# Performance work log

Measured on AMD Instinct MI355X. Metric: run time of the kernel, lower is better.

The kernel has to match this reference:

```python
import jax, jax.numpy as jnp
import numpy as np

NUM_HEADS = 8
WINDOW = 8


def setup_inputs() -> dict:
    key = jax.random.key(0)
    k1, k2, k3, k4 = jax.random.split(key, 4)
    B, H, W, C = 8, 192, 192, 192
    x = jax.random.normal(k1, (B, H * W, C), dtype=jnp.float32)
    w_qkv = jax.random.normal(k2, (C, 3 * C), dtype=jnp.float32) * 0.02
    w_proj = jax.random.normal(k3, (C, C), dtype=jnp.float32) * 0.02
    b_proj = jax.random.normal(k4, (C,), dtype=jnp.float32) * 0.02
    return {"x": x, "w_qkv": w_qkv, "w_proj": w_proj, "b_proj": b_proj, "H": H, "W": W}


def reference(x, w_qkv, w_proj, b_proj, H, W):
    B, L, C = x.shape
    N = WINDOW * WINDOW  # 64 tokens per window
    Nw = L // N          # number of windows (torch view chain == flat reshape, no permute)
    scale = (C // NUM_HEADS) ** -0.5
    # qkv projection on flat tokens, then window reshape
    qkv = (x @ w_qkv).reshape(B, Nw, N, 3, C)
    q = qkv[..., 0, :]
    k = qkv[..., 1, :] * scale
    v = qkv[..., 2, :]
    # channel attention: [B,Nw,C,C]
    attn = jnp.einsum('bwnc,bwnd->bwcd', k, v)
    attn = jax.nn.softmax(attn, axis=-1)
    # out[b,w,n,c] = sum_d attn[b,w,c,d] * q[b,w,n,d]
    out = jnp.einsum('bwcd,bwnd->bwnc', attn, q)
    out = out.reshape(B, L, C)
    return out @ w_proj + b_proj
```

## Files before the change

### kernel.cpp

```cpp
#include <hip/hip_runtime.h>
#include <hip/hip_bf16.h>

typedef short bf16x8 __attribute__((ext_vector_type(8)));
typedef float f32x4  __attribute__((ext_vector_type(4)));

__device__ __forceinline__ unsigned short f2bf(float f) {
  unsigned int u = __float_as_uint(f);
  u += 0x7fffu + ((u >> 16) & 1u);
  return (unsigned short)(u >> 16);
}

__device__ __forceinline__ f32x4 fzero() { f32x4 z = {0.f, 0.f, 0.f, 0.f}; return z; }

#define WQKV_FRAGS (6*36*64)
#define WP_FRAGS   (6*12*64)
#define WQKV_ELEMS (WQKV_FRAGS*8)

__global__ void prepack_weights(const float* __restrict__ wqkv,
                                const float* __restrict__ wproj,
                                unsigned short* __restrict__ ws) {
  int t = blockIdx.x * 256 + threadIdx.x;
  const float scale = 0.20412414523193154f;
  if (t < WQKV_FRAGS) {
    int kt  = t / (36*64);
    int rem = t - kt*(36*64);
    int nt  = rem >> 6;
    int l   = rem & 63;
    int n   = nt*16 + (l & 15);
    int k0  = kt*32 + (l >> 4)*8;
    float s = (n >= 192 && n < 384) ? scale : 1.0f;
    union { unsigned short us[8]; uint4 v; } u;
#pragma unroll
    for (int j = 0; j < 8; ++j) u.us[j] = f2bf(wqkv[(k0 + j)*576 + n] * s);
    *(uint4*)(ws + (size_t)t * 8) = u.v;
  } else if (t < WQKV_FRAGS + WP_FRAGS) {
    int t2  = t - WQKV_FRAGS;
    int kt  = t2 / (12*64);
    int rem = t2 - kt*(12*64);
    int nt  = rem >> 6;
    int l   = rem & 63;
    int n   = nt*16 + (l & 15);
    int k0  = kt*32 + (l >> 4)*8;
    union { unsigned short us[8]; uint4 v; } u;
#pragma unroll
    for (int j = 0; j < 8; ++j) u.us[j] = f2bf(wproj[(k0 + j)*192 + n]);
    *(uint4*)(ws + (size_t)WQKV_ELEMS + (size_t)t2 * 8) = u.v;
  }
}

__launch_bounds__(512, 2)
__global__ void win_attn_fused(const float* __restrict__ x,
                               const unsigned short* __restrict__ wqkv_sw,
                               const unsigned short* __restrict__ wp_sw,
                               const float* __restrict__ bias,
                               float* __restrict__ out) {
  __shared__ __align__(16) unsigned char smem[156672];
  unsigned short* sX    = (unsigned short*)(smem);
  unsigned short* sQ    = (unsigned short*)(smem + 25600);
  unsigned short* sKt   = (unsigned short*)(smem + 51200);
  unsigned short* sVt   = (unsigned short*)(smem + 78848);
  float*          sAttn = (float*)(smem + 106496);
  unsigned short* sOut  = (unsigned short*)(smem);

  const int tid  = threadIdx.x;
  const int lane = tid & 63;
  const int wv   = tid >> 6;
  const int l16  = lane & 15;
  const int lq   = lane >> 4;

  {
    const float4* xg = (const float4*)(x + (size_t)blockIdx.x * 12288);
#pragma unroll
    for (int i = 0; i < 6; ++i) {
      int idx = tid + i * 512;
      float4 v = xg[idx];
      int e = idx << 2;
      unsigned short* p = sX + (e / 192) * 200 + (e % 192);
      p[0] = f2bf(v.x); p[1] = f2bf(v.y); p[2] = f2bf(v.z); p[3] = f2bf(v.w);
    }
  }
  __syncthreads();

  {
    bf16x8 af[4][6];
#pragma unroll
    for (int ms = 0; ms < 4; ++ms)
#pragma unroll
      for (int kt = 0; kt < 6; ++kt)
        af[ms][kt] = *(const bf16x8*)(sX + (ms*16 + l16)*200 + kt*32 + lq*8);

    for (int nt = wv; nt < 36; nt += 8) {
      f32x4 acc[4] = {fzero(), fzero(), fzero(), fzero()};
      const bf16x8* bp = (const bf16x8*)wqkv_sw + nt*64 + lane;
#pragma unroll
      for (int kt = 0; kt < 6; ++kt) {
        bf16x8 b = bp[kt * (36*64)];
#pragma unroll
        for (int ms = 0; ms < 4; ++ms)
          acc[ms] = __builtin_amdgcn_mfma_f32_16x16x32_bf16(af[ms][kt], b, acc[ms], 0, 0, 0);
      }
      int c = nt*16 + l16;
#pragma unroll
      for (int ms = 0; ms < 4; ++ms) {
        int rb = ms*16 + lq*4;
        if (c < 192) {
#pragma unroll
          for (int r = 0; r < 4; ++r) sQ[(rb + r)*200 + c] = f2bf(acc[ms][r]);
        } else if (c < 384) {
#pragma unroll
          for (int r = 0; r < 4; ++r) sKt[(c - 192)*72 + rb + r] = f2bf(acc[ms][r]);
        } else {
#pragma unroll
          for (int r = 0; r < 4; ++r) sVt[(c - 384)*72 + rb + r] = f2bf(acc[ms][r]);
        }
      }
    }
  }
  __syncthreads();

  f32x4 accF[2][4];
#pragma unroll
  for (int s = 0; s < 2; ++s)
#pragma unroll
    for (int m = 0; m < 4; ++m) accF[s][m] = fzero();

  for (int cb = 0; cb < 3; ++cb) {
    {
      bf16x8 ak[4][2];
#pragma unroll
      for (int ms = 0; ms < 4; ++ms)
#pragma unroll
        for (int kt = 0; kt < 2; ++kt)
          ak[ms][kt] = *(const bf16x8*)(sKt + (cb*64 + ms*16 + l16)*72 + kt*32 + lq*8);
      for (int dt = wv; dt < 12; dt += 8) {
        f32x4 acc[4] = {fzero(), fzero(), fzero(), fzero()};
#pragma unroll
        for (int kt = 0; kt < 2; ++kt) {
          bf16x8 b = *(const bf16x8*)(sVt + (dt*16 + l16)*72 + kt*32 + lq*8);
#pragma unroll
          for (int ms = 0; ms < 4; ++ms)
            acc[ms] = __builtin_amdgcn_mfma_f32_16x16x32_bf16(ak[ms][kt], b, acc[ms], 0, 0, 0);
        }
        int d = dt*16 + l16;
#pragma unroll
        for (int ms = 0; ms < 4; ++ms)
#pragma unroll
          for (int r = 0; r < 4; ++r)
            sAttn[(ms*16 + lq*4 + r)*196 + d] = acc[ms][r];
      }
    }
    __syncthreads();

    {
      int row = tid >> 3, seg = tid & 7;
      float* rp = sAttn + row*196 + seg*24;
      float v0[24];
      float mx = -3.0e38f;
#pragma unroll
      for (int i = 0; i < 24; ++i) { v0[i] = rp[i]; mx = fmaxf(mx, v0[i]); }
      mx = fmaxf(mx, __shfl_xor(mx, 1));
      mx = fmaxf(mx, __shfl_xor(mx, 2));
      mx = fmaxf(mx, __shfl_xor(mx, 4));
      float s = 0.f;
#pragma unroll
      for (int i = 0; i < 24; ++i) { float e = __expf(v0[i] - mx); v0[i] = e; s += e; }
      s += __shfl_xor(s, 1);
      s += __shfl_xor(s, 2);
      s += __shfl_xor(s, 4);
      float inv = 1.0f / s;
#pragma unroll
      for (int i = 0; i < 24; ++i) rp[i] = v0[i] * inv;
    }
    __syncthreads();

    {
      int ct = wv & 3, mh = wv >> 2;
      bf16x8 aq[2][6];
#pragma unroll
      for (int mi = 0; mi < 2; ++mi)
#pragma unroll
        for (int kt = 0; kt < 6; ++kt)
          aq[mi][kt] = *(const bf16x8*)(sQ + ((mh*2 + mi)*16 + l16)*200 + kt*32 + lq*8);
      f32x4 acc[2] = {fzero(), fzero()};
#pragma unroll
      for (int kt = 0; kt < 6; ++kt) {
        const float* ap = sAttn + (ct*16 + l16)*196 + kt*32 + lq*8;
        float4 f0 = *(const float4*)ap;
        float4 f1 = *(const float4*)(ap + 4);
        bf16x8 b;
        b[0] = (short)f2bf(f0.x); b[1] = (short)f2bf(f0.y);
        b[2] = (short)f2bf(f0.z); b[3] = (short)f2bf(f0.w);
        b[4] = (short)f2bf(f1.x); b[5] = (short)f2bf(f1.y);
        b[6] = (short)f2bf(f1.z); b[7] = (short)f2bf(f1.w);
#pragma unroll
        for (int mi = 0; mi < 2; ++mi)
          acc[mi] = __builtin_amdgcn_mfma_f32_16x16x32_bf16(aq[mi][kt], b, acc[mi], 0, 0, 0);
      }
#pragma unroll
      for (int mi = 0; mi < 2; ++mi)
#pragma unroll
        for (int r = 0; r < 4; ++r)
          sOut[((mh*2 + mi)*16 + lq*4 + r)*72 + ct*16 + l16] = f2bf(acc[mi][r]);
    }
    __syncthreads();

    {
      bf16x8 ao[4][2];
#pragma unroll
      for (int ms = 0; ms < 4; ++ms)
#pragma unroll
        for (int kt = 0; kt < 2; ++kt)
          ao[ms][kt] = *(const bf16x8*)(sOut + (ms*16 + l16)*72 + kt*32 + lq*8);
#pragma unroll
      for (int slot = 0; slot < 2; ++slot) {
        int nt = wv + slot*8;
        if (nt < 12) {
          const bf16x8* bp = (const bf16x8*)wp_sw + ((cb*2)*12 + nt)*64 + lane;
#pragma unroll
          for (int kt = 0; kt < 2; ++kt) {
            bf16x8 b = bp[kt * (12*64)];
#pragma unroll
            for (int ms = 0; ms < 4; ++ms)
              accF[slot][ms] = __builtin_amdgcn_mfma_f32_16x16x32_bf16(ao[ms][kt], b, accF[slot][ms], 0, 0, 0);
          }
        }
      }
    }
  }

  {
    float* op = out + (size_t)blockIdx.x * 12288;
#pragma unroll
    for (int slot = 0; slot < 2; ++slot) {
      int nt = wv + slot*8;
      if (nt < 12) {
        int e = nt*16 + l16;
        float bv = bias[e];
#pragma unroll
        for (int ms = 0; ms < 4; ++ms)
#pragma unroll
          for (int r = 0; r < 4; ++r)
            op[(ms*16 + lq*4 + r)*192 + e] = accF[slot][ms][r] + bv;
      }
    }
  }
}

extern "C" void kernel_launch(void* const* d_in, const int* in_sizes, int n_in,
                              void* d_out, int out_size, void* d_ws, size_t ws_size,
                              hipStream_t stream) {
  const float* x     = (const float*)d_in[0];
  const float* wqkv  = (const float*)d_in[1];
  const float* wproj = (const float*)d_in[2];
  const float* bproj = (const float*)d_in[3];
  unsigned short* ws = (unsigned short*)d_ws;

  int nwin = in_sizes[0] / 12288;

  prepack_weights<<<72, 256, 0, stream>>>(wqkv, wproj, ws);
  win_attn_fused<<<nwin, 512, 0, stream>>>(x, ws, ws + WQKV_ELEMS, bproj, (float*)d_out);
}
```

Before: 591.2 us.

## Restructure channel attention into single pass with deferred softmax normalization

Replaces the three-chunk loop over channel blocks with one pass. Each wave computes a 96x48 slice of the K^T V scores in registers, exponentiates them without max subtraction, and produces row sums via shuffles and a small shared reduction. The 1/sum scale is applied after the attention-times-Q product. That product is shuffled straight into MFMA fragments for the output projection, with the two halves combined in shared memory and written out as coalesced float4 stores. This cuts shared-memory traffic, the fp32 attention buffer and barriers, and shrinks LDS. Dropping the max subtraction risks exp overflow for large logits.

Result: no change. 599.8 us (+1.5%).

```diff
diff --git a/kernel.cpp b/kernel.cpp
--- a/kernel.cpp
+++ b/kernel.cpp
@@ -1,5 +1,4 @@
 #include <hip/hip_runtime.h>
-#include <hip/hip_bf16.h>
 
 typedef short bf16x8 __attribute__((ext_vector_type(8)));
 typedef float f32x4  __attribute__((ext_vector_type(4)));
@@ -9,8 +8,8 @@
   u += 0x7fffu + ((u >> 16) & 1u);
   return (unsigned short)(u >> 16);
 }
-
-__device__ __forceinline__ f32x4 fzero() { f32x4 z = {0.f, 0.f, 0.f, 0.f}; return z; }
+__device__ __forceinline__ short f2bfs(float f) { return (short)f2bf(f); }
+__device__ __forceinline__ f32x4 fzero() { f32x4 z = {0.f,0.f,0.f,0.f}; return z; }
 
 #define WQKV_FRAGS (6*36*64)
 #define WP_FRAGS   (6*12*64)
@@ -22,8 +21,8 @@
   int t = blockIdx.x * 256 + threadIdx.x;
   const float scale = 0.20412414523193154f;
   if (t < WQKV_FRAGS) {
-    int kt  = t / (36*64);
-    int rem = t - kt*(36*64);
+    int kt  = t / 2304;
+    int rem = t - kt*2304;
     int nt  = rem >> 6;
     int l   = rem & 63;
     int n   = nt*16 + (l & 15);
@@ -34,16 +33,16 @@
     for (int j = 0; j < 8; ++j) u.us[j] = f2bf(wqkv[(k0 + j)*576 + n] * s);
     *(uint4*)(ws + (size_t)t * 8) = u.v;
   } else if (t < WQKV_FRAGS + WP_FRAGS) {
-    int t2  = t - WQKV_FRAGS;
-    int kt  = t2 / (12*64);
-    int rem = t2 - kt*(12*64);
-    int nt  = rem >> 6;
-    int l   = rem & 63;
-    int n   = nt*16 + (l & 15);
-    int k0  = kt*32 + (l >> 4)*8;
+    int t2   = t - WQKV_FRAGS;
+    int kt2g = t2 / 768;
+    int rem  = t2 - kt2g*768;
+    int ms2  = rem >> 6;
+    int l    = rem & 63;
+    int e    = ms2*16 + (l & 15);
+    int cc0  = kt2g*32 + (l >> 4)*8;
     union { unsigned short us[8]; uint4 v; } u;
 #pragma unroll
-    for (int j = 0; j < 8; ++j) u.us[j] = f2bf(wproj[(k0 + j)*192 + n]);
+    for (int j = 0; j < 8; ++j) u.us[j] = f2bf(wproj[(cc0 + j)*192 + e]);
     *(uint4*)(ws + (size_t)WQKV_ELEMS + (size_t)t2 * 8) = u.v;
   }
 }
@@ -54,20 +53,26 @@
                                const unsigned short* __restrict__ wp_sw,
                                const float* __restrict__ bias,
                                float* __restrict__ out) {
-  __shared__ __align__(16) unsigned char smem[156672];
-  unsigned short* sX    = (unsigned short*)(smem);
-  unsigned short* sQ    = (unsigned short*)(smem + 25600);
-  unsigned short* sKt   = (unsigned short*)(smem + 51200);
-  unsigned short* sVt   = (unsigned short*)(smem + 78848);
-  float*          sAttn = (float*)(smem + 106496);
-  unsigned short* sOut  = (unsigned short*)(smem);
+  __shared__ __align__(16) unsigned char smem[107264];
+  unsigned short* sX   = (unsigned short*)(smem);
+  unsigned short* sKt  = (unsigned short*)(smem + 25600);
+  unsigned short* sVt  = (unsigned short*)(smem + 53248);
+  unsigned short* sQ   = (unsigned short*)(smem + 80896);
+  unsigned short* sAtt = (unsigned short*)(smem);
+  float* sSum  = (float*)(smem + 76800);
+  float* sInv  = (float*)(smem + 79872);
+  float* sEpi  = (float*)(smem);
+  float* sBias = (float*)(smem + 106496);
 
   const int tid  = threadIdx.x;
   const int lane = tid & 63;
   const int wv   = tid >> 6;
   const int l16  = lane & 15;
   const int lq   = lane >> 4;
-
+  const int h    = wv >> 2;
+  const int q    = wv & 3;
+
+  if (tid < 192) sBias[tid] = bias[tid];
   {
     const float4* xg = (const float4*)(x + (size_t)blockIdx.x * 12288);
 #pragma unroll
@@ -76,7 +81,9 @@
       float4 v = xg[idx];
       int e = idx << 2;
       unsigned short* p = sX + (e / 192) * 200 + (e % 192);
-      p[0] = f2bf(v.x); p[1] = f2bf(v.y); p[2] = f2bf(v.z); p[3] = f2bf(v.w);
+      union { unsigned short us[4]; unsigned long long d; } u;
+      u.us[0]=f2bf(v.x); u.us[1]=f2bf(v.y); u.us[2]=f2bf(v.z); u.us[3]=f2bf(v.w);
+      *(unsigned long long*)p = u.d;
     }
   }
   __syncthreads();
@@ -94,7 +101,7 @@
       const bf16x8* bp = (const bf16x8*)wqkv_sw + nt*64 + lane;
 #pragma unroll
       for (int kt = 0; kt < 6; ++kt) {
-        bf16x8 b = bp[kt * (36*64)];
+        bf16x8 b = bp[kt * 2304];
 #pragma unroll
         for (int ms = 0; ms < 4; ++ms)
           acc[ms] = __builtin_amdgcn_mfma_f32_16x16x32_bf16(af[ms][kt], b, acc[ms], 0, 0, 0);
@@ -118,130 +125,160 @@
   }
   __syncthreads();
 
-  f32x4 accF[2][4];
-#pragma unroll
-  for (int s = 0; s < 2; ++s)
-#pragma unroll
-    for (int m = 0; m < 4; ++m) accF[s][m] = fzero();
-
-  for (int cb = 0; cb < 3; ++cb) {
-    {
-      bf16x8 ak[4][2];
-#pragma unroll
-      for (int ms = 0; ms < 4; ++ms)
-#pragma unroll
-        for (int kt = 0; kt < 2; ++kt)
-          ak[ms][kt] = *(const bf16x8*)(sKt + (cb*64 + ms*16 + l16)*72 + kt*32 + lq*8);
-      for (int dt = wv; dt < 12; dt += 8) {
-        f32x4 acc[4] = {fzero(), fzero(), fzero(), fzero()};
-#pragma unroll
-        for (int kt = 0; kt < 2; ++kt) {
-          bf16x8 b = *(const bf16x8*)(sVt + (dt*16 + l16)*72 + kt*32 + lq*8);
-#pragma unroll
-          for (int ms = 0; ms < 4; ++ms)
-            acc[ms] = __builtin_amdgcn_mfma_f32_16x16x32_bf16(ak[ms][kt], b, acc[ms], 0, 0, 0);
-        }
-        int d = dt*16 + l16;
-#pragma unroll
-        for (int ms = 0; ms < 4; ++ms)
-#pragma unroll
-          for (int r = 0; r < 4; ++r)
-            sAttn[(ms*16 + lq*4 + r)*196 + d] = acc[ms][r];
-      }
-    }
-    __syncthreads();
-
-    {
-      int row = tid >> 3, seg = tid & 7;
-      float* rp = sAttn + row*196 + seg*24;
-      float v0[24];
-      float mx = -3.0e38f;
-#pragma unroll
-      for (int i = 0; i < 24; ++i) { v0[i] = rp[i]; mx = fmaxf(mx, v0[i]); }
-      mx = fmaxf(mx, __shfl_xor(mx, 1));
-      mx = fmaxf(mx, __shfl_xor(mx, 2));
-      mx = fmaxf(mx, __shfl_xor(mx, 4));
-      float s = 0.f;
-#pragma unroll
-      for (int i = 0; i < 24; ++i) { float e = __expf(v0[i] - mx); v0[i] = e; s += e; }
-      s += __shfl_xor(s, 1);
-      s += __shfl_xor(s, 2);
-      s += __shfl_xor(s, 4);
-      float inv = 1.0f / s;
-#pragma unroll
-      for (int i = 0; i < 24; ++i) rp[i] = v0[i] * inv;
-    }
-    __syncthreads();
-
-    {
-      int ct = wv & 3, mh = wv >> 2;
-      bf16x8 aq[2][6];
-#pragma unroll
-      for (int mi = 0; mi < 2; ++mi)
-#pragma unroll
-        for (int kt = 0; kt < 6; ++kt)
-          aq[mi][kt] = *(const bf16x8*)(sQ + ((mh*2 + mi)*16 + l16)*200 + kt*32 + lq*8);
-      f32x4 acc[2] = {fzero(), fzero()};
-#pragma unroll
-      for (int kt = 0; kt < 6; ++kt) {
-        const float* ap = sAttn + (ct*16 + l16)*196 + kt*32 + lq*8;
-        float4 f0 = *(const float4*)ap;
-        float4 f1 = *(const float4*)(ap + 4);
-        bf16x8 b;
-        b[0] = (short)f2bf(f0.x); b[1] = (short)f2bf(f0.y);
-        b[2] = (short)f2bf(f0.z); b[3] = (short)f2bf(f0.w);
-        b[4] = (short)f2bf(f1.x); b[5] = (short)f2bf(f1.y);
-        b[6] = (short)f2bf(f1.z); b[7] = (short)f2bf(f1.w);
-#pragma unroll
-        for (int mi = 0; mi < 2; ++mi)
-          acc[mi] = __builtin_amdgcn_mfma_f32_16x16x32_bf16(aq[mi][kt], b, acc[mi], 0, 0, 0);
-      }
-#pragma unroll
-      for (int mi = 0; mi < 2; ++mi)
+  f32x4 acc2[6][3];
+  float p24[24];
+  {
+    bf16x8 ak[6][2];
+#pragma unroll
+    for (int ms = 0; ms < 6; ++ms)
+#pragma unroll
+      for (int kt = 0; kt < 2; ++kt)
+        ak[ms][kt] = *(const bf16x8*)(sKt + (h*96 + ms*16 + l16)*72 + kt*32 + lq*8);
+#pragma unroll
+    for (int ms = 0; ms < 6; ++ms)
+#pragma unroll
+      for (int dc = 0; dc < 3; ++dc) acc2[ms][dc] = fzero();
+#pragma unroll
+    for (int dc = 0; dc < 3; ++dc) {
+      int dt = q + dc*4;
+      bf16x8 bv[2];
+#pragma unroll
+      for (int kt = 0; kt < 2; ++kt)
+        bv[kt] = *(const bf16x8*)(sVt + (dt*16 + l16)*72 + kt*32 + lq*8);
+#pragma unroll
+      for (int kt = 0; kt < 2; ++kt)
+#pragma unroll
+        for (int ms = 0; ms < 6; ++ms)
+          acc2[ms][dc] = __builtin_amdgcn_mfma_f32_16x16x32_bf16(ak[ms][kt], bv[kt], acc2[ms][dc], 0, 0, 0);
+    }
+#pragma unroll
+    for (int ms = 0; ms < 6; ++ms)
+#pragma unroll
+      for (int dc = 0; dc < 3; ++dc)
+#pragma unroll
+        for (int r = 0; r < 4; ++r) acc2[ms][dc][r] = __expf(acc2[ms][dc][r]);
+#pragma unroll
+    for (int ms = 0; ms < 6; ++ms)
+#pragma unroll
+      for (int r = 0; r < 4; ++r) {
+        float s = acc2[ms][0][r] + acc2[ms][1][r] + acc2[ms][2][r];
+        s += __shfl_xor(s, 1); s += __shfl_xor(s, 2);
+        s += __shfl_xor(s, 4); s += __shfl_xor(s, 8);
+        p24[ms*4 + r] = s;
+      }
+  }
+  __syncthreads();
+
+  {
+#pragma unroll
+    for (int ms = 0; ms < 6; ++ms) {
+      int cc = h*96 + ms*16 + lq*4;
+#pragma unroll
+      for (int dc = 0; dc < 3; ++dc) {
+        int d = (q + dc*4)*16 + l16;
 #pragma unroll
         for (int r = 0; r < 4; ++r)
-          sOut[((mh*2 + mi)*16 + lq*4 + r)*72 + ct*16 + l16] = f2bf(acc[mi][r]);
-    }
-    __syncthreads();
-
-    {
-      bf16x8 ao[4][2];
-#pragma unroll
-      for (int ms = 0; ms < 4; ++ms)
-#pragma unroll
-        for (int kt = 0; kt < 2; ++kt)
-          ao[ms][kt] = *(const bf16x8*)(sOut + (ms*16 + l16)*72 + kt*32 + lq*8);
-#pragma unroll
-      for (int slot = 0; slot < 2; ++slot) {
-        int nt = wv + slot*8;
-        if (nt < 12) {
-          const bf16x8* bp = (const bf16x8*)wp_sw + ((cb*2)*12 + nt)*64 + lane;
-#pragma unroll
-          for (int kt = 0; kt < 2; ++kt) {
-            bf16x8 b = bp[kt * (12*64)];
-#pragma unroll
-            for (int ms = 0; ms < 4; ++ms)
-              accF[slot][ms] = __builtin_amdgcn_mfma_f32_16x16x32_bf16(ao[ms][kt], b, accF[slot][ms], 0, 0, 0);
-          }
-        }
-      }
-    }
-  }
+          sAtt[(cc + r)*200 + d] = f2bf(acc2[ms][dc][r]);
+      }
+    }
+    if (l16 == 0) {
+#pragma unroll
+      for (int ms = 0; ms < 6; ++ms)
+#pragma unroll
+        for (int r = 0; r < 4; ++r)
+          sSum[(h*96 + ms*16 + lq*4 + r)*4 + q] = p24[ms*4 + r];
+    }
+  }
+  __syncthreads();
+
+  if (tid < 192) {
+    float s = sSum[tid*4] + sSum[tid*4+1] + sSum[tid*4+2] + sSum[tid*4+3];
+    sInv[tid] = 1.0f / s;
+  }
+
+  f32x4 acc3[6];
+#pragma unroll
+  for (int ms = 0; ms < 6; ++ms) acc3[ms] = fzero();
+#pragma unroll
+  for (int kt = 0; kt < 6; ++kt) {
+    bf16x8 bq = *(const bf16x8*)(sQ + (q*16 + l16)*200 + kt*32 + lq*8);
+#pragma unroll
+    for (int ms = 0; ms < 6; ++ms) {
+      bf16x8 a = *(const bf16x8*)(sAtt + (h*96 + ms*16 + l16)*200 + kt*32 + lq*8);
+      acc3[ms] = __builtin_amdgcn_mfma_f32_16x16x32_bf16(a, bq, acc3[ms], 0, 0, 0);
+    }
+  }
+  __syncthreads();
+
+#pragma unroll
+  for (int ms = 0; ms < 6; ++ms) {
+    f32x4 inv = *(const f32x4*)(sInv + h*96 + ms*16 + lq*4);
+#pragma unroll
+    for (int r = 0; r < 4; ++r) acc3[ms][r] *= inv[r];
+  }
+
+  f32x4 accF[12];
+#pragma unroll
+  for (int m = 0; m < 12; ++m) accF[m] = fzero();
+  {
+    bf16x8 bfr[3];
+    const int srcBase = l16 + ((lq & 1) << 5);
+    const bool hiSel = (lq >= 2);
+#pragma unroll
+    for (int kt2 = 0; kt2 < 3; ++kt2) {
+#pragma unroll
+      for (int j = 0; j < 8; ++j) {
+        int srcLane = srcBase + ((j >> 2) << 4);
+        float va = __shfl(acc3[2*kt2][j & 3], srcLane);
+        float vb = __shfl(acc3[2*kt2 + 1][j & 3], srcLane);
+        bfr[kt2][j] = f2bfs(hiSel ? vb : va);
+      }
+    }
+    const bf16x8* wpb = (const bf16x8*)wp_sw;
+#pragma unroll
+    for (int ms2 = 0; ms2 < 12; ++ms2) {
+#pragma unroll
+      for (int kt2 = 0; kt2 < 3; ++kt2) {
+        bf16x8 wa = wpb[((3*h + kt2)*12 + ms2)*64 + lane];
+        accF[ms2] = __builtin_amdgcn_mfma_f32_16x16x32_bf16(wa, bfr[kt2], accF[ms2], 0, 0, 0);
+      }
+    }
+  }
+
+  if (h == 0) {
+#pragma unroll
+    for (int ms2 = 0; ms2 < 12; ++ms2) {
+      int e0 = ms2*16 + lq*4;
+      f32x4 b4 = *(const f32x4*)(sBias + e0);
+      f32x4 v = accF[ms2];
+#pragma unroll
+      for (int r = 0; r < 4; ++r) v[r] += b4[r];
+      *(f32x4*)(sEpi + (q*16 + l16)*200 + e0) = v;
+    }
+  }
+  __syncthreads();
+  if (h == 1) {
+#pragma unroll
+    for (int ms2 = 0; ms2 < 12; ++ms2) {
+      int e0 = ms2*16 + lq*4;
+      float* p = sEpi + (q*16 + l16)*200 + e0;
+      f32x4 v = *(f32x4*)p;
+#pragma unroll
+      for (int r = 0; r < 4; ++r) v[r] += accF[ms2][r];
+      *(f32x4*)p = v;
+    }
+  }
+  __syncthreads();
 
   {
     float* op = out + (size_t)blockIdx.x * 12288;
 #pragma unroll
-    for (int slot = 0; slot < 2; ++slot) {
-      int nt = wv + slot*8;
-      if (nt < 12) {
-        int e = nt*16 + l16;
-        float bv = bias[e];
-#pragma unroll
-        for (int ms = 0; ms < 4; ++ms)
-#pragma unroll
-          for (int r = 0; r < 4; ++r)
-            op[(ms*16 + lq*4 + r)*192 + e] = accF[slot][ms][r] + bv;
-      }
+    for (int i = 0; i < 6; ++i) {
+      int s = tid + i*512;
+      int token = s / 48;
+      int e4 = s - token*48;
+      f32x4 v = *(const f32x4*)(sEpi + token*200 + e4*4);
+      *(f32x4*)(op + s*4) = v;
     }
   }
 }
```
